# Kernel optimization log

Measured on AMD Instinct MI355X. Metric: run time of the kernel, lower is better.

## Reference

```python
import jax, jax.numpy as jnp
import numpy as np
from jax import lax

THRESH = 0.8
LENS = 0.4
DECAY = 0.2
LOG_SIG_MIN, LOG_SIG_MAX = -20.0, 2.0
WINS = 15

@jax.custom_vjp
def act_fun(x):
    return (x > THRESH).astype(x.dtype)

def _act_fwd(x):
    return act_fun(x), x

def _act_bwd(x, g):
    return (g * (jnp.abs(x - THRESH) < LENS).astype(g.dtype),)

act_fun.defvjp(_act_fwd, _act_bwd)

B, NIN, HID, NACT = 2048, 512, 1024, 32

def _xavier(key, out_d, in_d):
    lim = jnp.sqrt(6.0 / (in_d + out_d)).astype(jnp.float32)
    return jax.random.uniform(key, (out_d, in_d), jnp.float32, -lim, lim)

def setup_inputs() -> dict:
    key = jax.random.key(0)
    ks = jax.random.split(key, 12)
    inp = {
        'state': jax.random.normal(ks[0], (B, 5, NIN), jnp.float32),
        'w1': _xavier(ks[1], HID, NIN), 'b1': jnp.zeros((HID,), jnp.float32),
        'w2': _xavier(ks[2], HID, NIN), 'b2': jnp.zeros((HID,), jnp.float32),
        'w3': _xavier(ks[3], HID, NIN), 'b3': jnp.zeros((HID,), jnp.float32),
        'wl': _xavier(ks[4], 1, 3), 'bl': jnp.zeros((1,), jnp.float32),
        'w11': _xavier(ks[5], HID, 4 * HID), 'b11': jnp.zeros((HID,), jnp.float32),
        'w12': _xavier(ks[6], HID, HID), 'b12': jnp.zeros((HID,), jnp.float32),
        'w21': _xavier(ks[7], HID, 4 * HID), 'b21': jnp.zeros((HID,), jnp.float32),
        'w22': _xavier(ks[8], HID, HID), 'b22': jnp.zeros((HID,), jnp.float32),
        'wm': _xavier(ks[9], NACT, HID), 'bm': jnp.zeros((NACT,), jnp.float32),
        'ws': _xavier(ks[10], NACT, HID), 'bs': jnp.zeros((NACT,), jnp.float32),
    }
    return inp

def _policy_forward(state, w1, b1, w2, b2, w3, b3, wl, bl,
                    w11, b11, w12, b12, w21, b21, w22, b22, wm, bm, ws, bs):
    batch = state.shape[0]
    hid = w1.shape[0]
    seq = jnp.repeat(state, 3, axis=1)
    mem0 = jnp.zeros((batch, hid, 4), state.dtype)
    sp0 = jnp.zeros((batch, hid, 4), state.dtype)

    def step(carry, x_t):
        mem, spike = carry
        i1 = x_t @ w1.T + b1  # [B, HID]
        i2 = x_t @ w2.T + b2
        i3 = x_t @ w3.T + b3
        inner = jnp.einsum('bck,k->bc', mem[:, :, :3], wl[0]) + bl[0]
        inp_all = jnp.stack([i1, i2, i3, inner], axis=-1)  # [B, HID, 4]
        mem1 = mem * DECAY * (1.0 - spike) + inp_all
        sp1 = act_fun(mem1)
        return (mem1, sp1), sp1

    _, spikes = lax.scan(step, (mem0, sp0), jnp.swapaxes(seq, 0, 1))  # [T,B,HID,4]
    spikes = jnp.transpose(spikes, (1, 0, 2, 3)).reshape(batch, WINS, hid * 4)
    x = jnp.mean(spikes, axis=1)  # [B, 4*HID]

    x1 = jax.nn.relu(x @ w11.T + b11)
    x1 = jax.nn.relu(x1 @ w12.T + b12)
    mean = x1 @ wm.T + bm

    x2 = jax.nn.relu(x @ w21.T + b21)
    x2 = jax.nn.relu(x2 @ w22.T + b22)
    log_std = jnp.clip(x2 @ ws.T + bs, LOG_SIG_MIN, LOG_SIG_MAX)
    return mean, log_std

def reference(state, w1, b1, w2, b2, w3, b3, wl, bl,
              w11, b11, w12, b12, w21, b21, w22, b22, wm, bm, ws, bs):
    return _policy_forward(state, w1, b1, w2, b2, w3, b3, wl, bl,
                           w11, b11, w12, b12, w21, b21, w22, b22, wm, bm, ws, bs)
```

## Files before the change

### kernel.cpp

```cpp
#include <hip/hip_runtime.h>
#include <cstddef>
#include <cstdint>

#define THRESH 0.8f
#define DECAY  0.2f

typedef unsigned short ushort_t;
typedef __attribute__((ext_vector_type(8))) short bf16x8;
typedef __attribute__((ext_vector_type(4))) float f32x4;
typedef __attribute__((ext_vector_type(4))) int i32x4;

__device__ __forceinline__ ushort_t f2bf(float f) {
    union { float f; unsigned u; } v; v.f = f;
    unsigned r = v.u + 0x7FFFu + ((v.u >> 16) & 1u);
    return (ushort_t)(r >> 16);
}
__device__ __forceinline__ float bf2f(ushort_t h) {
    union { unsigned u; float f; } v; v.u = ((unsigned)h) << 16;
    return v.f;
}
__device__ __forceinline__ float blo(unsigned u) {
    union { unsigned x; float f; } v; v.x = u << 16; return v.f;
}
__device__ __forceinline__ float bhi(unsigned u) {
    union { unsigned x; float f; } v; v.x = u & 0xFFFF0000u; return v.f;
}

__device__ __forceinline__ void gload16(const void* g, void* l) {
    __builtin_amdgcn_global_load_lds(
        (const __attribute__((address_space(1))) void*)g,
        (__attribute__((address_space(3))) void*)l,
        16, 0, 0);
}

#define DSREAD(dst, addr, off) \
    asm volatile("ds_read_b128 %0, %1 offset:" #off : "=v"(dst) : "v"(addr))

#define MM(i, j, a, w) \
    acc[i][j] = __builtin_amdgcn_mfma_f32_16x16x32_bf16(a, w, acc[i][j], 0, 0, 0)

__global__ __launch_bounds__(512, 4) void fused_cur_lif(
    const ushort_t* __restrict__ A, const ushort_t* __restrict__ W,
    const float* __restrict__ b123, const float* __restrict__ wl,
    const float* __restrict__ bl, signed char* __restrict__ xb)
{
    __shared__ ushort_t lds[3][11264];

    const int t = threadIdx.x;
    const int bx = blockIdx.x;
    const int by = blockIdx.y;
    const int lane = t & 63;
    const int wv = t >> 6;
    const int wm = (wv >> 2) * 80;
    const int wn = (wv & 3) * 48;
    const int fr = lane & 15;
    const int fq = lane >> 4;
    const int swz16 = (fq ^ ((fr >> 1) & 3)) * 16;

    const unsigned av0 = (unsigned)((wm + fr) * 64 + swz16);
    const unsigned av1 = av0 + 22528;
    const unsigned av2 = av0 + 45056;
    const unsigned bv0 = (unsigned)(10240 + (wn + fr) * 64 + swz16);
    const unsigned bv1 = bv0 + 22528;
    const unsigned bv2 = bv0 + 45056;

    const ushort_t* src0; const ushort_t* src1;
    const ushort_t* src2; const ushort_t* src3;
    int dst0, dst1, dst2, dst3;
    if (wv < 5) {
        const int rl0 = wv * 32 + (lane >> 2);
        const int rl1 = rl0 + 16;
        src0 = A + (size_t)(bx * 160 + rl0) * 1536 + ((lane & 3) ^ ((rl0 >> 1) & 3)) * 8;
        src1 = A + (size_t)(bx * 160 + rl1) * 1536 + ((lane & 3) ^ ((rl1 >> 1) & 3)) * 8;
        src2 = src0; src3 = src1;
        dst0 = rl0 * 32 + (lane & 3) * 8;
        dst1 = rl1 * 32 + (lane & 3) * 8;
        dst2 = dst0; dst3 = dst1;
    } else {
        const int rb = (wv - 5) * 64 + (lane >> 2);
        src0 = W + (size_t)(by * 192 + rb) * 1536 + ((lane & 3) ^ ((rb >> 1) & 3)) * 8;
        src1 = src0 + (size_t)16 * 1536;
        src2 = src0 + (size_t)32 * 1536;
        src3 = src0 + (size_t)48 * 1536;
        dst0 = 5120 + rb * 32 + (lane & 3) * 8;
        dst1 = dst0 + 16 * 32;
        dst2 = dst0 + 32 * 32;
        dst3 = dst0 + 48 * 32;
    }

#define STAGE(tile, sbuf)                                              \
    do {                                                               \
        ushort_t* lb_ = &lds[sbuf][0];                                 \
        if (wv < 5) {                                                  \
            gload16(src0 + (tile) * 32, lb_ + dst0);                   \
            gload16(src1 + (tile) * 32, lb_ + dst1);                   \
        } else {                                                       \
            gload16(src0 + (tile) * 32, lb_ + dst0);                   \
            gload16(src1 + (tile) * 32, lb_ + dst1);                   \
            gload16(src2 + (tile) * 32, lb_ + dst2);                   \
            gload16(src3 + (tile) * 32, lb_ + dst3);                   \
        }                                                              \
    } while (0)

#define COMPUTE(av_, bv_)                                              \
    do {                                                               \
        bf16x8 af0, af1, af2, af3, af4, wf0, wf1, wf2;                 \
        DSREAD(af0, av_, 0);                                           \
        DSREAD(af1, av_, 1024);                                        \
        DSREAD(af2, av_, 2048);                                        \
        DSREAD(af3, av_, 3072);                                        \
        DSREAD(af4, av_, 4096);                                        \
        DSREAD(wf0, bv_, 0);                                           \
        DSREAD(wf1, bv_, 1024);                                        \
        DSREAD(wf2, bv_, 2048);                                        \
        asm volatile("s_waitcnt lgkmcnt(0)" ::: "memory");             \
        __builtin_amdgcn_sched_barrier(0);                             \
        __builtin_amdgcn_s_setprio(1);                                 \
        MM(0, 0, af0, wf0); MM(0, 1, af0, wf1); MM(0, 2, af0, wf2);    \
        MM(1, 0, af1, wf0); MM(1, 1, af1, wf1); MM(1, 2, af1, wf2);    \
        MM(2, 0, af2, wf0); MM(2, 1, af2, wf1); MM(2, 2, af2, wf2);    \
        MM(3, 0, af3, wf0); MM(3, 1, af3, wf1); MM(3, 2, af3, wf2);    \
        MM(4, 0, af4, wf0); MM(4, 1, af4, wf1); MM(4, 2, af4, wf2);    \
        __builtin_amdgcn_s_setprio(0);                                 \
    } while (0)

    f32x4 acc[5][3];
#pragma unroll
    for (int i = 0; i < 5; i++)
#pragma unroll
        for (int j = 0; j < 3; j++) {
            f32x4 z = {0.f, 0.f, 0.f, 0.f};
            acc[i][j] = z;
        }

    STAGE(0, 0);
    STAGE(1, 1);

#pragma unroll
    for (int tt = 0; tt < 46; ++tt) {
        STAGE(tt + 2, (tt + 2) % 3);
        if (wv < 5) asm volatile("s_waitcnt vmcnt(4)" ::: "memory");
        else        asm volatile("s_waitcnt vmcnt(8)" ::: "memory");
        __builtin_amdgcn_s_barrier();
        __builtin_amdgcn_sched_barrier(0);
        const unsigned av_ = (tt % 3 == 0) ? av0 : (tt % 3 == 1) ? av1 : av2;
        const unsigned bv_ = (tt % 3 == 0) ? bv0 : (tt % 3 == 1) ? bv1 : bv2;
        COMPUTE(av_, bv_);
        __builtin_amdgcn_s_barrier();
        __builtin_amdgcn_sched_barrier(0);
    }
    if (wv < 5) asm volatile("s_waitcnt vmcnt(2)" ::: "memory");
    else        asm volatile("s_waitcnt vmcnt(4)" ::: "memory");
    __builtin_amdgcn_s_barrier();
    __builtin_amdgcn_sched_barrier(0);
    COMPUTE(av1, bv1);
    __builtin_amdgcn_s_barrier();
    __builtin_amdgcn_sched_barrier(0);
    asm volatile("s_waitcnt vmcnt(0)" ::: "memory");
    __builtin_amdgcn_s_barrier();
    __builtin_amdgcn_sched_barrier(0);
    COMPUTE(av2, bv2);
#undef STAGE
#undef COMPUTE

    const int ch = by * 64 + (wv & 3) * 16 + fr;
    const float b1c = b123[ch];
    const float b2c = b123[1024 + ch];
    const float b3c = b123[2048 + ch];
    const float wl0 = wl[0], wl1 = wl[1], wl2 = wl[2], bl0 = bl[0];
    const int bbase = bx * 32 + (wv >> 2) * 16 + fq * 4;
#pragma unroll
    for (int r = 0; r < 4; r++) {
        float m0 = 0.f, m1 = 0.f, m2 = 0.f, m3 = 0.f;
        int s0 = 0, s1 = 0, s2 = 0, s3 = 0;
#pragma unroll
        for (int f = 0; f < 5; f++) {
            const float i1 = acc[f][0][r] + b1c;
            const float i2 = acc[f][1][r] + b2c;
            const float i3 = acc[f][2][r] + b3c;
#pragma unroll
            for (int rep = 0; rep < 3; rep++) {
                const float inner = m0 * wl0 + m1 * wl1 + m2 * wl2 + bl0;
                const float n0 = i1 + ((m0 > THRESH) ? 0.f : DECAY * m0);
                const float n1 = i2 + ((m1 > THRESH) ? 0.f : DECAY * m1);
                const float n2 = i3 + ((m2 > THRESH) ? 0.f : DECAY * m2);
                const float n3 = inner + ((m3 > THRESH) ? 0.f : DECAY * m3);
                m0 = n0; m1 = n1; m2 = n2; m3 = n3;
                s0 += (n0 > THRESH); s1 += (n1 > THRESH);
                s2 += (n2 > THRESH); s3 += (n3 > THRESH);
            }
        }
        uchar4 o;
        o.x = (unsigned char)s0; o.y = (unsigned char)s1;
        o.z = (unsigned char)s2; o.w = (unsigned char)s3;
        *(uchar4*)&xb[(size_t)(bbase + r) * 4096 + ch * 4] = o;
    }
}

__global__ __launch_bounds__(256, 2) void mlp1_i8(
    const signed char* __restrict__ A, const signed char* __restrict__ W,
    const float* __restrict__ wsc, const float* __restrict__ bias,
    ushort_t* __restrict__ C)
{
    __shared__ signed char lds[3][12288];

    const int t = threadIdx.x;
    const int mBase = blockIdx.x * 64;
    const int nBase = blockIdx.y * 128;

    const int lane = t & 63;
    const int wv = t >> 6;
    const int wn = wv * 32;
    const int fr = lane & 15;
    const int fq = lane >> 4;
    const int fsw = (fq ^ ((fr >> 1) & 3)) * 16;

    const unsigned a0 = (unsigned)(fr * 64 + fsw);
    const unsigned a1 = a0 + 12288, a2 = a0 + 24576;
    const unsigned b0 = (unsigned)(4096 + (wn + fr) * 64 + fsw);
    const unsigned b1 = b0 + 12288, b2 = b0 + 24576;

    const int r0 = t >> 2;
    const int cc = ((t & 3) ^ ((r0 >> 1) & 3)) * 16;
    const signed char* srcA  = A + (size_t)(mBase + r0) * 4096 + cc;
    const signed char* srcW0 = W + (size_t)(nBase + r0) * 4096 + cc;
    const signed char* srcW1 = W + (size_t)(nBase + 64 + r0) * 4096 + cc;

#define STAGE1(tile)                                                   \
    do {                                                               \
        signed char* lb_ = &lds[(tile) % 3][0];                        \
        gload16(srcA  + (tile) * 64, lb_ + t * 16);                    \
        gload16(srcW0 + (tile) * 64, lb_ + 4096 + t * 16);             \
        gload16(srcW1 + (tile) * 64, lb_ + 8192 + t * 16);             \
    } while (0)

#define COMPUTE1(av_, bv_)                                             \
    do {                                                               \
        i32x4 af0, af1, af2, af3, wf0, wf1;                            \
        DSREAD(af0, av_, 0);                                           \
        DSREAD(af1, av_, 1024);                                        \
        DSREAD(af2, av_, 2048);                                        \
        DSREAD(af3, av_, 3072);                                        \
        DSREAD(wf0, bv_, 0);                                           \
        DSREAD(wf1, bv_, 1024);                                        \
        asm volatile("s_waitcnt lgkmcnt(0)" ::: "memory");             \
        __builtin_amdgcn_sched_barrier(0);                             \
        __builtin_amdgcn_s_setprio(1);                                 \
        acc[0][0] = __builtin_amdgcn_mfma_i32_16x16x64_i8(af0, wf0, acc[0][0], 0, 0, 0); \
        acc[0][1] = __builtin_amdgcn_mfma_i32_16x16x64_i8(af0, wf1, acc[0][1], 0, 0, 0); \
        acc[1][0] = __builtin_amdgcn_mfma_i32_16x16x64_i8(af1, wf0, acc[1][0], 0, 0, 0); \
        acc[1][1] = __builtin_amdgcn_mfma_i32_16x16x64_i8(af1, wf1, acc[1][1], 0, 0, 0); \
        acc[2][0] = __builtin_amdgcn_mfma_i32_16x16x64_i8(af2, wf0, acc[2][0], 0, 0, 0); \
        acc[2][1] = __builtin_amdgcn_mfma_i32_16x16x64_i8(af2, wf1, acc[2][1], 0, 0, 0); \
        acc[3][0] = __builtin_amdgcn_mfma_i32_16x16x64_i8(af3, wf0, acc[3][0], 0, 0, 0); \
        acc[3][1] = __builtin_amdgcn_mfma_i32_16x16x64_i8(af3, wf1, acc[3][1], 0, 0, 0); \
        __builtin_amdgcn_s_setprio(0);                                 \
    } while (0)

    i32x4 acc[4][2];
#pragma unroll
    for (int i = 0; i < 4; i++)
#pragma unroll
        for (int j = 0; j < 2; j++) {
            i32x4 z = {0, 0, 0, 0};
            acc[i][j] = z;
        }

    STAGE1(0);
    STAGE1(1);

#pragma unroll
    for (int tt = 0; tt < 62; ++tt) {
        STAGE1(tt + 2);
        asm volatile("s_waitcnt vmcnt(6)" ::: "memory");
        __builtin_amdgcn_s_barrier();
        __builtin_amdgcn_sched_barrier(0);
        const unsigned av_ = (tt % 3 == 0) ? a0 : (tt % 3 == 1) ? a1 : a2;
        const unsigned bv_ = (tt % 3 == 0) ? b0 : (tt % 3 == 1) ? b1 : b2;
        COMPUTE1(av_, bv_);
        __builtin_amdgcn_s_barrier();
        __builtin_amdgcn_sched_barrier(0);
    }
    asm volatile("s_waitcnt vmcnt(3)" ::: "memory");
    __builtin_amdgcn_s_barrier();
    __builtin_amdgcn_sched_barrier(0);
    COMPUTE1(a2, b2);
    __builtin_amdgcn_s_barrier();
    __builtin_amdgcn_sched_barrier(0);
    asm volatile("s_waitcnt vmcnt(0)" ::: "memory");
    __builtin_amdgcn_s_barrier();
    __builtin_amdgcn_sched_barrier(0);
    COMPUTE1(a0, b0);
#undef STAGE1
#undef COMPUTE1

#pragma unroll
    for (int j = 0; j < 2; j++) {
        const int col = nBase + wn + j * 16 + fr;
        const float sc = wsc[col];
        const float bv = bias[col];
#pragma unroll
        for (int i = 0; i < 4; i++)
#pragma unroll
            for (int r = 0; r < 4; r++) {
                const int row = mBase + i * 16 + fq * 4 + r;
                const float v = (float)acc[i][j][r] * sc + bv;
                C[(size_t)row * 2048 + col] = f2bf(fmaxf(v, 0.f));
            }
    }
}

__global__ __launch_bounds__(256, 2) void mlp2_bf16(
    const ushort_t* __restrict__ A, const ushort_t* __restrict__ W,
    const float* __restrict__ bias, ushort_t* __restrict__ C,
    int N, int K, int lda, int ldw, int ldc, int aHalfOff)
{
    __shared__ ushort_t lds[3][6144];

    const int t = threadIdx.x;
    const int mBase = blockIdx.x * 64;
    const int nBase = blockIdx.y * 128;
    const int aOff = (2 * nBase >= N) ? aHalfOff : 0;

    const int lane = t & 63;
    const int wv = t >> 6;
    const int wn = wv * 32;
    const int fr = lane & 15;
    const int fq = lane >> 4;
    const int fsw = (fq ^ ((fr >> 1) & 3)) * 16;

    const unsigned a0 = (unsigned)(fr * 64 + fsw);
    const unsigned a1 = a0 + 12288, a2 = a0 + 24576;
    const unsigned b0 = (unsigned)(4096 + (wn + fr) * 64 + fsw);
    const unsigned b1 = b0 + 12288, b2 = b0 + 24576;

    const int r0 = t >> 2;
    const int cc = ((t & 3) ^ ((r0 >> 1) & 3)) * 8;
    const ushort_t* srcA  = A + (size_t)(mBase + r0) * lda + aOff + cc;
    const ushort_t* srcW0 = W + (size_t)(nBase + r0) * ldw + cc;
    const ushort_t* srcW1 = W + (size_t)(nBase + 64 + r0) * ldw + cc;

#define STAGE2(tile)                                                   \
    do {                                                               \
        char* lb_ = (char*)&lds[(tile) % 3][0];                        \
        gload16(srcA  + (tile) * 32, lb_ + t * 16);                    \
        gload16(srcW0 + (tile) * 32, lb_ + 4096 + t * 16);             \
        gload16(srcW1 + (tile) * 32, lb_ + 8192 + t * 16);             \
    } while (0)

#define COMPUTE2(av_, bv_)                                             \
    do {                                                               \
        bf16x8 af0, af1, af2, af3, wf0, wf1;                           \
        DSREAD(af0, av_, 0);                                           \
        DSREAD(af1, av_, 1024);                                        \
        DSREAD(af2, av_, 2048);                                        \
        DSREAD(af3, av_, 3072);                                        \
        DSREAD(wf0, bv_, 0);                                           \
        DSREAD(wf1, bv_, 1024);                                        \
        asm volatile("s_waitcnt lgkmcnt(0)" ::: "memory");             \
        __builtin_amdgcn_sched_barrier(0);                             \
        __builtin_amdgcn_s_setprio(1);                                 \
        MM(0, 0, af0, wf0); MM(0, 1, af0, wf1);                        \
        MM(1, 0, af1, wf0); MM(1, 1, af1, wf1);                        \
        MM(2, 0, af2, wf0); MM(2, 1, af2, wf1);                        \
        MM(3, 0, af3, wf0); MM(3, 1, af3, wf1);                        \
        __builtin_amdgcn_s_setprio(0);                                 \
    } while (0)

    f32x4 acc[4][2];
#pragma unroll
    for (int i = 0; i < 4; i++)
#pragma unroll
        for (int j = 0; j < 2; j++) {
            f32x4 z = {0.f, 0.f, 0.f, 0.f};
            acc[i][j] = z;
        }

    STAGE2(0);
    STAGE2(1);

#pragma unroll
    for (int tt = 0; tt < 30; ++tt) {
        STAGE2(tt + 2);
        asm volatile("s_waitcnt vmcnt(6)" ::: "memory");
        __builtin_amdgcn_s_barrier();
        __builtin_amdgcn_sched_barrier(0);
        const unsigned av_ = (tt % 3 == 0) ? a0 : (tt % 3 == 1) ? a1 : a2;
        const unsigned bv_ = (tt % 3 == 0) ? b0 : (tt % 3 == 1) ? b1 : b2;
        COMPUTE2(av_, bv_);
        __builtin_amdgcn_s_barrier();
        __builtin_amdgcn_sched_barrier(0);
    }
    asm volatile("s_waitcnt vmcnt(3)" ::: "memory");
    __builtin_amdgcn_s_barrier();
    __builtin_amdgcn_sched_barrier(0);
    COMPUTE2(a0, b0);
    __builtin_amdgcn_s_barrier();
    __builtin_amdgcn_sched_barrier(0);
    asm volatile("s_waitcnt vmcnt(0)" ::: "memory");
    __builtin_amdgcn_s_barrier();
    __builtin_amdgcn_sched_barrier(0);
    COMPUTE2(a1, b1);
#undef STAGE2
#undef COMPUTE2

#pragma unroll
    for (int j = 0; j < 2; j++) {
        const int col = nBase + wn + j * 16 + fr;
        const float bv = bias[col];
#pragma unroll
        for (int i = 0; i < 4; i++)
#pragma unroll
            for (int r = 0; r < 4; r++) {
                const int row = mBase + i * 16 + fq * 4 + r;
                C[(size_t)row * ldc + col] = f2bf(fmaxf(acc[i][j][r] + bv, 0.f));
            }
    }
}

__device__ __forceinline__ void split_state_perm(const float4* src, ushort4* dst,
                                                 int base, int t) {
#pragma unroll
    for (int p = 0; p < 4; p++) {
        const int i = base * 1024 + p * 256 + t;
        const float4 v = src[i];
        ushort4 h, l;
        h.x = f2bf(v.x); l.x = f2bf(v.x - bf2f(h.x));
        h.y = f2bf(v.y); l.y = f2bf(v.y - bf2f(h.y));
        h.z = f2bf(v.z); l.z = f2bf(v.z - bf2f(h.z));
        h.w = f2bf(v.w); l.w = f2bf(v.w - bf2f(h.w));
        const int s = i >> 7, c4 = i & 127;
        const int b = s / 5, f = s - b * 5;
        const int m = ((b >> 5) * 160) + (((b >> 4) & 1) * 80) + (f << 4) + (b & 15);
        ushort4* row = dst + (size_t)m * 384;
        row[c4] = h; row[128 + c4] = h; row[256 + c4] = l;
    }
}
__device__ __forceinline__ void split_w_perm(const float4* src, ushort4* dst,
                                             int base, int t, int j) {
#pragma unroll
    for (int p = 0; p < 4; p++) {
        const int i = base * 1024 + p * 256 + t;
        const float4 v = src[i];
        ushort4 h, l;
        h.x = f2bf(v.x); l.x = f2bf(v.x - bf2f(h.x));
        h.y = f2bf(v.y); l.y = f2bf(v.y - bf2f(h.y));
        h.z = f2bf(v.z); l.z = f2bf(v.z - bf2f(h.z));
        h.w = f2bf(v.w); l.w = f2bf(v.w - bf2f(h.w));
        const int c = i >> 7, c4 = i & 127;
        const int n = ((c >> 6) * 192) + (((c >> 4) & 3) * 48) + (j << 4) + (c & 15);
        ushort4* row = dst + (size_t)n * 384;
        row[c4] = h; row[128 + c4] = l; row[256 + c4] = h;
    }
}
__device__ __forceinline__ void do_cvt4(const float4* src, ushort4* dst,
                                        int base, int t) {
#pragma unroll
    for (int p = 0; p < 4; p++) {
        const int i = base * 1024 + p * 256 + t;
        const float4 v = src[i];
        ushort4 h;
        h.x = f2bf(v.x); h.y = f2bf(v.y); h.z = f2bf(v.z); h.w = f2bf(v.w);
        dst[i] = h;
    }
}
__device__ __forceinline__ int q8(float x, float inv) {
    int q = (int)rintf(x * inv);
    q = q > 127 ? 127 : (q < -127 ? -127 : q);
    return q & 0xff;
}

__global__ __launch_bounds__(256) void prep_kernel(
    const float* __restrict__ state,
    const float* __restrict__ w1, const float* __restrict__ w2,
    const float* __restrict__ w3,
    const float* __restrict__ w11, const float* __restrict__ w21,
    const float* __restrict__ w12, const float* __restrict__ w22,
    const float* __restrict__ b1, const float* __restrict__ b2,
    const float* __restrict__ b3, const float* __restrict__ b11,
    const float* __restrict__ b21, const float* __restrict__ b12,
    const float* __restrict__ b22,
    ushort_t* __restrict__ Ap, ushort_t* __restrict__ Wp,
    signed char* __restrict__ w1q, float* __restrict__ wsc,
    ushort_t* __restrict__ w2b,
    float* __restrict__ b123, float* __restrict__ bb1, float* __restrict__ bb2)
{
    const int bid = blockIdx.x;
    const int t = threadIdx.x;
    if (bid < 1280) {
        split_state_perm((const float4*)state, (ushort4*)Ap, bid, t);
    } else if (bid < 1408) {
        split_w_perm((const float4*)w1, (ushort4*)Wp, bid - 1280, t, 0);
    } else if (bid < 1536) {
        split_w_perm((const float4*)w2, (ushort4*)Wp, bid - 1408, t, 1);
    } else if (bid < 1664) {
        split_w_perm((const float4*)w3, (ushort4*)Wp, bid - 1536, t, 2);
    } else if (bid < 3712) {
        const int r = bid - 1664;
        const float* src = (r < 1024) ? (w11 + (size_t)r * 4096)
                                      : (w21 + (size_t)(r - 1024) * 4096);
        __shared__ float red4[4];
        float4 v[4];
        float lmax = 0.f;
#pragma unroll
        for (int p = 0; p < 4; p++) {
            v[p] = ((const float4*)src)[t * 4 + p];
            lmax = fmaxf(lmax, fmaxf(fmaxf(fabsf(v[p].x), fabsf(v[p].y)),
                                     fmaxf(fabsf(v[p].z), fabsf(v[p].w))));
        }
#pragma unroll
        for (int d = 1; d < 64; d <<= 1)
            lmax = fmaxf(lmax, __shfl_xor(lmax, d, 64));
        if ((t & 63) == 0) red4[t >> 6] = lmax;
        __syncthreads();
        const float gmax = fmaxf(fmaxf(fmaxf(red4[0], red4[1]),
                                       fmaxf(red4[2], red4[3])), 1e-30f);
        const float inv = 127.0f / gmax;
        int4 o;
        o.x = q8(v[0].x, inv) | (q8(v[0].y, inv) << 8) | (q8(v[0].z, inv) << 16) | (q8(v[0].w, inv) << 24);
        o.y = q8(v[1].x, inv) | (q8(v[1].y, inv) << 8) | (q8(v[1].z, inv) << 16) | (q8(v[1].w, inv) << 24);
        o.z = q8(v[2].x, inv) | (q8(v[2].y, inv) << 8) | (q8(v[2].z, inv) << 16) | (q8(v[2].w, inv) << 24);
        o.w = q8(v[3].x, inv) | (q8(v[3].y, inv) << 8) | (q8(v[3].z, inv) << 16) | (q8(v[3].w, inv) << 24);
        ((int4*)(w1q + (size_t)r * 4096))[t] = o;
        if (t == 0) wsc[r] = gmax / (127.0f * 15.0f);
    } else if (bid < 3968) {
        do_cvt4((const float4*)w12, (ushort4*)w2b, bid - 3712, t);
    } else if (bid < 4224) {
        do_cvt4((const float4*)w22, (ushort4*)(w2b + 1048576), bid - 3968, t);
    } else {
#pragma unroll
        for (int p = 0; p < 4; p++) {
            const int i = p * 256 + t;
            b123[i] = b1[i]; b123[1024 + i] = b2[i]; b123[2048 + i] = b3[i];
            bb1[i] = b11[i]; bb1[1024 + i] = b21[i];
            bb2[i] = b12[i]; bb2[1024 + i] = b22[i];
        }
    }
}

__global__ __launch_bounds__(256) void head_kernel(
    const ushort_t* __restrict__ h, const float* __restrict__ wm,
    const float* __restrict__ bm, const float* __restrict__ ws,
    const float* __restrict__ bs, float* __restrict__ out)
{
    const int t = threadIdx.x;
    const int branch = blockIdx.x >> 8;
    const int n = t & 31;
    const int b = (blockIdx.x & 255) * 8 + (t >> 5);
    const ushort_t* hr = h + (size_t)b * 2048 + branch * 1024;
    const float* wr = (branch ? ws : wm) + (size_t)n * 1024;
    float s = 0.f;
#pragma unroll 4
    for (int k = 0; k < 1024; k += 8) {
        const uint4 hv = *(const uint4*)&hr[k];
        const float4 w0 = *(const float4*)&wr[k];
        const float4 w1 = *(const float4*)&wr[k + 4];
        s += blo(hv.x) * w0.x + bhi(hv.x) * w0.y
           + blo(hv.y) * w0.z + bhi(hv.y) * w0.w
           + blo(hv.z) * w1.x + bhi(hv.z) * w1.y
           + blo(hv.w) * w1.z + bhi(hv.w) * w1.w;
    }
    s += (branch ? bs : bm)[n];
    if (branch) s = fminf(fmaxf(s, -20.f), 2.f);
    out[(size_t)branch * 65536 + (size_t)b * 32 + n] = s;
}

extern "C" void kernel_launch(void* const* d_in, const int* in_sizes, int n_in,
                              void* d_out, int out_size, void* d_ws, size_t ws_size,
                              hipStream_t stream)
{
    const float* state = (const float*)d_in[0];
    const float* w1  = (const float*)d_in[1];  const float* b1  = (const float*)d_in[2];
    const float* w2  = (const float*)d_in[3];  const float* b2  = (const float*)d_in[4];
    const float* w3  = (const float*)d_in[5];  const float* b3  = (const float*)d_in[6];
    const float* wl  = (const float*)d_in[7];  const float* bl  = (const float*)d_in[8];
    const float* w11 = (const float*)d_in[9];  const float* b11 = (const float*)d_in[10];
    const float* w12 = (const float*)d_in[11]; const float* b12 = (const float*)d_in[12];
    const float* w21 = (const float*)d_in[13]; const float* b21 = (const float*)d_in[14];
    const float* w22 = (const float*)d_in[15]; const float* b22 = (const float*)d_in[16];
    const float* wm  = (const float*)d_in[17]; const float* bm  = (const float*)d_in[18];
    const float* ws  = (const float*)d_in[19]; const float* bs  = (const float*)d_in[20];
    float* out = (float*)d_out;

    char* wp = (char*)d_ws;
    ushort_t*    Ap    = (ushort_t*)wp;    wp += (size_t)10240 * 1536 * 2;
    ushort_t*    Wp    = (ushort_t*)wp;    wp += (size_t)3072 * 1536 * 2;
    signed char* xb    = (signed char*)wp; wp += (size_t)2048 * 4096;
    signed char* w1q   = (signed char*)wp; wp += (size_t)2048 * 4096;
    ushort_t*    w2b   = (ushort_t*)wp;    wp += (size_t)2048 * 1024 * 2;
    ushort_t*    h1    = (ushort_t*)wp;    wp += (size_t)2048 * 2048 * 2;
    ushort_t*    h2    = (ushort_t*)wp;    wp += (size_t)2048 * 2048 * 2;
    float*       wsc   = (float*)wp;       wp += 2048 * 4;
    float*       b123  = (float*)wp;       wp += 3072 * 4;
    float*       bb1   = (float*)wp;       wp += 2048 * 4;
    float*       bb2   = (float*)wp;       wp += 2048 * 4;

    prep_kernel<<<4225, 256, 0, stream>>>(
        state, w1, w2, w3, w11, w21, w12, w22,
        b1, b2, b3, b11, b21, b12, b22,
        Ap, Wp, w1q, wsc, w2b, b123, bb1, bb2);

    fused_cur_lif<<<dim3(64, 16), 512, 0, stream>>>(Ap, Wp, b123, wl, bl, xb);

    mlp1_i8<<<dim3(32, 16), 256, 0, stream>>>(xb, w1q, wsc, bb1, h1);

    mlp2_bf16<<<dim3(32, 16), 256, 0, stream>>>(
        h1, w2b, bb2, h2, 2048, 1024, 2048, 1024, 2048, 1024);

    head_kernel<<<512, 256, 0, stream>>>(h2, wm, bm, ws, bs, out);
}
```

Before: 353.1 us.

## Shrink fused LIF GEMM block to 4 waves with larger per-wave tiles

Changes the fused current/LIF kernel from 8 waves of 80x48 tiles to 4 waves of 80x96 tiles per block. Each wave now holds twice the accumulators and reads six weight fragments per step, so the A fragments are reused across more MFMAs. Global-to-LDS staging is split evenly across waves, and the epilogue loops over two channel groups. This is meant to cut LDS read traffic per MFMA and barrier overhead. The cost is higher register pressure and fewer waves available to hide latency.

Measured after the change: 360.5 us. 1.02x slower.

```diff
diff --git a/kernel.cpp b/kernel.cpp
--- a/kernel.cpp
+++ b/kernel.cpp
@@ -39,7 +39,7 @@
 #define MM(i, j, a, w) \
     acc[i][j] = __builtin_amdgcn_mfma_f32_16x16x32_bf16(a, w, acc[i][j], 0, 0, 0)
 
-__global__ __launch_bounds__(512, 4) void fused_cur_lif(
+__global__ __launch_bounds__(256, 2) void fused_cur_lif(
     const ushort_t* __restrict__ A, const ushort_t* __restrict__ W,
     const float* __restrict__ b123, const float* __restrict__ wl,
     const float* __restrict__ bl, signed char* __restrict__ xb)
@@ -51,8 +51,8 @@
     const int by = blockIdx.y;
     const int lane = t & 63;
     const int wv = t >> 6;
-    const int wm = (wv >> 2) * 80;
-    const int wn = (wv & 3) * 48;
+    const int wm = (wv >> 1) * 80;
+    const int wn = (wv & 1) * 96;
     const int fr = lane & 15;
     const int fq = lane >> 4;
     const int swz16 = (fq ^ ((fr >> 1) & 3)) * 16;
@@ -64,71 +64,72 @@
     const unsigned bv1 = bv0 + 22528;
     const unsigned bv2 = bv0 + 45056;
 
-    const ushort_t* src0; const ushort_t* src1;
-    const ushort_t* src2; const ushort_t* src3;
-    int dst0, dst1, dst2, dst3;
-    if (wv < 5) {
-        const int rl0 = wv * 32 + (lane >> 2);
-        const int rl1 = rl0 + 16;
-        src0 = A + (size_t)(bx * 160 + rl0) * 1536 + ((lane & 3) ^ ((rl0 >> 1) & 3)) * 8;
-        src1 = A + (size_t)(bx * 160 + rl1) * 1536 + ((lane & 3) ^ ((rl1 >> 1) & 3)) * 8;
-        src2 = src0; src3 = src1;
-        dst0 = rl0 * 32 + (lane & 3) * 8;
-        dst1 = rl1 * 32 + (lane & 3) * 8;
-        dst2 = dst0; dst3 = dst1;
-    } else {
-        const int rb = (wv - 5) * 64 + (lane >> 2);
-        src0 = W + (size_t)(by * 192 + rb) * 1536 + ((lane & 3) ^ ((rb >> 1) & 3)) * 8;
-        src1 = src0 + (size_t)16 * 1536;
-        src2 = src0 + (size_t)32 * 1536;
-        src3 = src0 + (size_t)48 * 1536;
-        dst0 = 5120 + rb * 32 + (lane & 3) * 8;
-        dst1 = dst0 + 16 * 32;
-        dst2 = dst0 + 32 * 32;
-        dst3 = dst0 + 48 * 32;
-    }
+    const int half = wv >> 1;
+    const int idx2 = (wv & 1) * 64 + lane;
+    const ushort_t* gbase = (half == 0) ? A : W;
+    const int rbase = (half == 0) ? bx * 160 : by * 192;
+    const int lbase = (half == 0) ? 0 : 5120;
+    const ushort_t* gs0; const ushort_t* gs1; const ushort_t* gs2;
+    const ushort_t* gs3; const ushort_t* gs4; const ushort_t* gs5;
+    int ld0, ld1, ld2, ld3, ld4, ld5;
+#define MKSRC(q, GS, LD)                                                   \
+    {                                                                      \
+        const int slot = (q) * 128 + idx2;                                 \
+        const int row = slot >> 2, chk = slot & 3;                         \
+        GS = gbase + (size_t)(rbase + row) * 1536 +                        \
+             (chk ^ ((row >> 1) & 3)) * 8;                                 \
+        LD = lbase + row * 32 + chk * 8;                                   \
+    }
+    MKSRC(0, gs0, ld0) MKSRC(1, gs1, ld1) MKSRC(2, gs2, ld2)
+    MKSRC(3, gs3, ld3) MKSRC(4, gs4, ld4) MKSRC(5, gs5, ld5)
+#undef MKSRC
 
 #define STAGE(tile, sbuf)                                              \
     do {                                                               \
         ushort_t* lb_ = &lds[sbuf][0];                                 \
-        if (wv < 5) {                                                  \
-            gload16(src0 + (tile) * 32, lb_ + dst0);                   \
-            gload16(src1 + (tile) * 32, lb_ + dst1);                   \
-        } else {                                                       \
-            gload16(src0 + (tile) * 32, lb_ + dst0);                   \
-            gload16(src1 + (tile) * 32, lb_ + dst1);                   \
-            gload16(src2 + (tile) * 32, lb_ + dst2);                   \
-            gload16(src3 + (tile) * 32, lb_ + dst3);                   \
-        }                                                              \
+        gload16(gs0 + (tile) * 32, lb_ + ld0);                         \
+        gload16(gs1 + (tile) * 32, lb_ + ld1);                         \
+        gload16(gs2 + (tile) * 32, lb_ + ld2);                         \
+        gload16(gs3 + (tile) * 32, lb_ + ld3);                         \
+        gload16(gs4 + (tile) * 32, lb_ + ld4);                         \
+        if (half) gload16(gs5 + (tile) * 32, lb_ + ld5);               \
     } while (0)
 
 #define COMPUTE(av_, bv_)                                              \
     do {                                                               \
-        bf16x8 af0, af1, af2, af3, af4, wf0, wf1, wf2;                 \
-        DSREAD(af0, av_, 0);                                           \
-        DSREAD(af1, av_, 1024);                                        \
-        DSREAD(af2, av_, 2048);                                        \
-        DSREAD(af3, av_, 3072);                                        \
-        DSREAD(af4, av_, 4096);                                        \
-        DSREAD(wf0, bv_, 0);                                           \
-        DSREAD(wf1, bv_, 1024);                                        \
-        DSREAD(wf2, bv_, 2048);                                        \
+        bf16x8 a0, a1, a2, a3, a4, w0, w1, w2, w3, w4, w5;             \
+        DSREAD(a0, av_, 0);                                            \
+        DSREAD(a1, av_, 1024);                                         \
+        DSREAD(a2, av_, 2048);                                         \
+        DSREAD(a3, av_, 3072);                                         \
+        DSREAD(a4, av_, 4096);                                         \
+        DSREAD(w0, bv_, 0);                                            \
+        DSREAD(w1, bv_, 1024);                                         \
+        DSREAD(w2, bv_, 2048);                                         \
+        DSREAD(w3, bv_, 3072);                                         \
+        DSREAD(w4, bv_, 4096);                                         \
+        DSREAD(w5, bv_, 5120);                                         \
         asm volatile("s_waitcnt lgkmcnt(0)" ::: "memory");             \
         __builtin_amdgcn_sched_barrier(0);                             \
         __builtin_amdgcn_s_setprio(1);                                 \
-        MM(0, 0, af0, wf0); MM(0, 1, af0, wf1); MM(0, 2, af0, wf2);    \
-        MM(1, 0, af1, wf0); MM(1, 1, af1, wf1); MM(1, 2, af1, wf2);    \
-        MM(2, 0, af2, wf0); MM(2, 1, af2, wf1); MM(2, 2, af2, wf2);    \
-        MM(3, 0, af3, wf0); MM(3, 1, af3, wf1); MM(3, 2, af3, wf2);    \
-        MM(4, 0, af4, wf0); MM(4, 1, af4, wf1); MM(4, 2, af4, wf2);    \
+        MM(0, 0, a0, w0); MM(0, 1, a0, w1); MM(0, 2, a0, w2);          \
+        MM(0, 3, a0, w3); MM(0, 4, a0, w4); MM(0, 5, a0, w5);          \
+        MM(1, 0, a1, w0); MM(1, 1, a1, w1); MM(1, 2, a1, w2);          \
+        MM(1, 3, a1, w3); MM(1, 4, a1, w4); MM(1, 5, a1, w5);          \
+        MM(2, 0, a2, w0); MM(2, 1, a2, w1); MM(2, 2, a2, w2);          \
+        MM(2, 3, a2, w3); MM(2, 4, a2, w4); MM(2, 5, a2, w5);          \
+        MM(3, 0, a3, w0); MM(3, 1, a3, w1); MM(3, 2, a3, w2);          \
+        MM(3, 3, a3, w3); MM(3, 4, a3, w4); MM(3, 5, a3, w5);          \
+        MM(4, 0, a4, w0); MM(4, 1, a4, w1); MM(4, 2, a4, w2);          \
+        MM(4, 3, a4, w3); MM(4, 4, a4, w4); MM(4, 5, a4, w5);          \
         __builtin_amdgcn_s_setprio(0);                                 \
     } while (0)
 
-    f32x4 acc[5][3];
+    f32x4 acc[5][6];
 #pragma unroll
     for (int i = 0; i < 5; i++)
 #pragma unroll
-        for (int j = 0; j < 3; j++) {
+        for (int j = 0; j < 6; j++) {
             f32x4 z = {0.f, 0.f, 0.f, 0.f};
             acc[i][j] = z;
         }
@@ -139,8 +140,8 @@
 #pragma unroll
     for (int tt = 0; tt < 46; ++tt) {
         STAGE(tt + 2, (tt + 2) % 3);
-        if (wv < 5) asm volatile("s_waitcnt vmcnt(4)" ::: "memory");
-        else        asm volatile("s_waitcnt vmcnt(8)" ::: "memory");
+        if (half == 0) asm volatile("s_waitcnt vmcnt(10)" ::: "memory");
+        else           asm volatile("s_waitcnt vmcnt(12)" ::: "memory");
         __builtin_amdgcn_s_barrier();
         __builtin_amdgcn_sched_barrier(0);
         const unsigned av_ = (tt % 3 == 0) ? av0 : (tt % 3 == 1) ? av1 : av2;
@@ -149,8 +150,8 @@
         __builtin_amdgcn_s_barrier();
         __builtin_amdgcn_sched_barrier(0);
     }
-    if (wv < 5) asm volatile("s_waitcnt vmcnt(2)" ::: "memory");
-    else        asm volatile("s_waitcnt vmcnt(4)" ::: "memory");
+    if (half == 0) asm volatile("s_waitcnt vmcnt(5)" ::: "memory");
+    else           asm volatile("s_waitcnt vmcnt(6)" ::: "memory");
     __builtin_amdgcn_s_barrier();
     __builtin_amdgcn_sched_barrier(0);
     COMPUTE(av1, bv1);
@@ -163,37 +164,41 @@
 #undef STAGE
 #undef COMPUTE
 
-    const int ch = by * 64 + (wv & 3) * 16 + fr;
-    const float b1c = b123[ch];
-    const float b2c = b123[1024 + ch];
-    const float b3c = b123[2048 + ch];
+    const int chBase = by * 64 + (wv & 1) * 32 + fr;
     const float wl0 = wl[0], wl1 = wl[1], wl2 = wl[2], bl0 = bl[0];
-    const int bbase = bx * 32 + (wv >> 2) * 16 + fq * 4;
-#pragma unroll
-    for (int r = 0; r < 4; r++) {
-        float m0 = 0.f, m1 = 0.f, m2 = 0.f, m3 = 0.f;
-        int s0 = 0, s1 = 0, s2 = 0, s3 = 0;
-#pragma unroll
-        for (int f = 0; f < 5; f++) {
-            const float i1 = acc[f][0][r] + b1c;
-            const float i2 = acc[f][1][r] + b2c;
-            const float i3 = acc[f][2][r] + b3c;
-#pragma unroll
-            for (int rep = 0; rep < 3; rep++) {
-                const float inner = m0 * wl0 + m1 * wl1 + m2 * wl2 + bl0;
-                const float n0 = i1 + ((m0 > THRESH) ? 0.f : DECAY * m0);
-                const float n1 = i2 + ((m1 > THRESH) ? 0.f : DECAY * m1);
-                const float n2 = i3 + ((m2 > THRESH) ? 0.f : DECAY * m2);
-                const float n3 = inner + ((m3 > THRESH) ? 0.f : DECAY * m3);
-                m0 = n0; m1 = n1; m2 = n2; m3 = n3;
-                s0 += (n0 > THRESH); s1 += (n1 > THRESH);
-                s2 += (n2 > THRESH); s3 += (n3 > THRESH);
+    const int bbase = bx * 32 + (wv >> 1) * 16 + fq * 4;
+#pragma unroll
+    for (int g = 0; g < 2; g++) {
+        const int ch = chBase + g * 16;
+        const float b1c = b123[ch];
+        const float b2c = b123[1024 + ch];
+        const float b3c = b123[2048 + ch];
+#pragma unroll
+        for (int r = 0; r < 4; r++) {
+            float m0 = 0.f, m1 = 0.f, m2 = 0.f, m3 = 0.f;
+            int s0 = 0, s1 = 0, s2 = 0, s3 = 0;
+#pragma unroll
+            for (int f = 0; f < 5; f++) {
+                const float i1 = acc[f][g * 3 + 0][r] + b1c;
+                const float i2 = acc[f][g * 3 + 1][r] + b2c;
+                const float i3 = acc[f][g * 3 + 2][r] + b3c;
+#pragma unroll
+                for (int rep = 0; rep < 3; rep++) {
+                    const float inner = m0 * wl0 + m1 * wl1 + m2 * wl2 + bl0;
+                    const float n0 = i1 + ((m0 > THRESH) ? 0.f : DECAY * m0);
+                    const float n1 = i2 + ((m1 > THRESH) ? 0.f : DECAY * m1);
+                    const float n2 = i3 + ((m2 > THRESH) ? 0.f : DECAY * m2);
+                    const float n3 = inner + ((m3 > THRESH) ? 0.f : DECAY * m3);
+                    m0 = n0; m1 = n1; m2 = n2; m3 = n3;
+                    s0 += (n0 > THRESH); s1 += (n1 > THRESH);
+                    s2 += (n2 > THRESH); s3 += (n3 > THRESH);
+                }
             }
+            uchar4 o;
+            o.x = (unsigned char)s0; o.y = (unsigned char)s1;
+            o.z = (unsigned char)s2; o.w = (unsigned char)s3;
+            *(uchar4*)&xb[(size_t)(bbase + r) * 4096 + ch * 4] = o;
         }
-        uchar4 o;
-        o.x = (unsigned char)s0; o.y = (unsigned char)s1;
-        o.z = (unsigned char)s2; o.w = (unsigned char)s3;
-        *(uchar4*)&xb[(size_t)(bbase + r) * 4096 + ch * 4] = o;
     }
 }
 
@@ -600,7 +605,7 @@
         b1, b2, b3, b11, b21, b12, b22,
         Ap, Wp, w1q, wsc, w2b, b123, bb1, bb2);
 
-    fused_cur_lif<<<dim3(64, 16), 512, 0, stream>>>(Ap, Wp, b123, wl, bl, xb);
+    fused_cur_lif<<<dim3(64, 16), 256, 0, stream>>>(Ap, Wp, b123, wl, bl, xb);
 
     mlp1_i8<<<dim3(32, 16), 256, 0, stream>>>(xb, w1q, wsc, bb1, h1);
 
```
